# Optimization experiments

Hardware: AMD Instinct MI355X
Metric: run time of the kernel (lower is better)

The kernel has to match this reference:

```python
import jax, jax.numpy as jnp
import numpy as np

N_NODES = 50000
N_EDGES = 800000
IN, HID, OUT = 128, 128, 64


def _mean_agg(h, src, dst, n):
    # gather source-node features along edges, segment-mean into destination nodes
    msgs = h[src]                                          # [E, d]
    summ = jax.ops.segment_sum(msgs, dst, num_segments=n)  # [N, d]
    deg = jax.ops.segment_sum(jnp.ones((src.shape[0],), h.dtype), dst, num_segments=n)
    return summ / jnp.maximum(deg, 1.0)[:, None]           # zero-in-degree -> 0


def _sage_layer(h, src, dst, W_self, W_neigh, b, n):
    # DGL SAGEConv mean: fc_self(h) + fc_neigh(mean_neigh(h)) + bias
    agg = _mean_agg(h, src, dst, n)
    return h @ W_self + agg @ W_neigh + b


def setup_inputs() -> dict:
    key = jax.random.key(0)
    ks = jax.random.split(key, 8)
    s = 1.0 / np.sqrt(IN)
    return {
        "feat": jax.random.normal(ks[0], (N_NODES, IN), jnp.float32),
        "src": jax.random.randint(ks[1], (N_EDGES,), 0, N_NODES, jnp.int64),
        "dst": jax.random.randint(ks[2], (N_EDGES,), 0, N_NODES, jnp.int64),
        "W_self1": jax.random.normal(ks[3], (IN, HID), jnp.float32) * s,
        "W_neigh1": jax.random.normal(ks[4], (IN, HID), jnp.float32) * s,
        "b1": jnp.zeros((HID,), jnp.float32),
        "W_self2": jax.random.normal(ks[5], (HID, OUT), jnp.float32) * (1.0 / np.sqrt(HID)),
        "W_neigh2": jax.random.normal(ks[6], (HID, OUT), jnp.float32) * (1.0 / np.sqrt(HID)),
        "b2": jnp.zeros((OUT,), jnp.float32),
    }


def reference(feat, src, dst, W_self1, W_neigh1, b1, W_self2, W_neigh2, b2):
    n = feat.shape[0]
    h = _sage_layer(feat, src, dst, W_self1, W_neigh1, b1, n)
    h = jax.nn.relu(h)  # dropout is identity in eval mode
    h = _sage_layer(h, src, dst, W_self2, W_neigh2, b2, n)
    return h
```

## Files before the change

### kernel.cpp

```cpp
#include <hip/hip_runtime.h>

#define N_NODES 50000
#define N_EDGES 800000

typedef unsigned short ushort_t;
typedef unsigned int uint_t;
typedef __attribute__((ext_vector_type(8))) short bf16x8;
typedef __attribute__((ext_vector_type(4))) float f32x4;

#define NB 196
#define BCAP 6144
#define SDEPTH 16
#define EPB 1024
#define NBLK_BUCKET ((N_EDGES + EPB - 1) / EPB)

#define IOFF_ROWPTR  100000
#define IOFF_EIDX    150016
#define IOFF_BBASE   950016
#define IOFF_BCNT    950528
#define UOFF_WT      1920000
#define UOFF_FEATB   2000000
#define UOFF_AGG1B   8400000
#define UOFF_H1B     14800000
#define UOFF_P2B     21200000

__device__ __forceinline__ float bf2f(uint_t u) {
    return __uint_as_float(u << 16);
}
__device__ __forceinline__ uint_t f2bf(float f) {
    uint_t x = __float_as_uint(f);
    return (x + 0x7FFFu + ((x >> 16) & 1u)) >> 16;
}

__global__ __launch_bounds__(256) void bucket_kernel(const int* __restrict__ src,
                                                     const int* __restrict__ dst,
                                                     uint_t* __restrict__ bucket,
                                                     int* __restrict__ bcnt) {
    __shared__ uint_t stage[NB][SDEPTH];
    __shared__ int lcnt[NB];
    __shared__ int gbase[NB];
    int tid = threadIdx.x;
    for (int i = tid; i < NB; i += 256) lcnt[i] = 0;
    __syncthreads();
    int e0 = blockIdx.x * EPB;
#pragma unroll
    for (int it = 0; it < EPB / 256; ++it) {
        int e = e0 + it * 256 + tid;
        if (e < N_EDGES) {
            int d = dst[e], s = src[e];
            uint_t v = ((uint_t)d << 16) | (uint_t)s;
            int b = d >> 8;
            int slot = atomicAdd(&lcnt[b], 1);
            if (slot < SDEPTH) {
                stage[b][slot] = v;
            } else {
                int p = atomicAdd(&bcnt[b], 1);
                bucket[(long)b * BCAP + p] = v;
            }
        }
    }
    __syncthreads();
    if (tid < NB) {
        int n = min(lcnt[tid], SDEPTH);
        gbase[tid] = (n > 0) ? atomicAdd(&bcnt[tid], n) : 0;
    }
    __syncthreads();
    for (int s = tid; s < NB * SDEPTH; s += 256) {
        int b = s >> 4, i = s & (SDEPTH - 1);
        if (i < min(lcnt[b], SDEPTH))
            bucket[(long)b * BCAP + gbase[b] + i] = stage[b][i];
    }
}

__global__ __launch_bounds__(256) void scan196(const int* __restrict__ bcnt,
                                               int* __restrict__ bbase,
                                               int* __restrict__ rowptr) {
    __shared__ int sh[256];
    int tid = threadIdx.x;
    int v = (tid < NB) ? bcnt[tid] : 0;
    sh[tid] = v;
    __syncthreads();
    for (int off = 1; off < 256; off <<= 1) {
        int t = (tid >= off) ? sh[tid - off] : 0;
        __syncthreads();
        sh[tid] += t;
        __syncthreads();
    }
    if (tid < NB) bbase[tid] = sh[tid] - v;
    if (tid == NB - 1) rowptr[N_NODES] = sh[tid];
}

__global__ __launch_bounds__(512) void fill_bucket(const uint_t* __restrict__ bucket,
                                                   const int* __restrict__ bcnt,
                                                   const int* __restrict__ bbase,
                                                   int* __restrict__ rowptr,
                                                   int* __restrict__ eidx) {
    __shared__ int hist[256];
    __shared__ int excl[256];
    __shared__ int fp[256];
    int b = blockIdx.x, tid = threadIdx.x;
    if (tid < 256) { hist[tid] = 0; fp[tid] = 0; }
    __syncthreads();
    int n = bcnt[b];
    int base = bbase[b];
    int nodebase = b << 8;
    const uint_t* bk = bucket + (long)b * BCAP;
    for (int i = tid; i < n; i += 512) {
        int d = (int)(bk[i] >> 16) - nodebase;
        atomicAdd(&hist[d], 1);
    }
    __syncthreads();
    int v = 0;
    if (tid < 256) { v = hist[tid]; excl[tid] = v; }
    __syncthreads();
    for (int off = 1; off < 256; off <<= 1) {
        int t = 0;
        if (tid < 256 && tid >= off) t = excl[tid - off];
        __syncthreads();
        if (tid < 256) excl[tid] += t;
        __syncthreads();
    }
    if (tid < 256) {
        excl[tid] -= v;
        int node = nodebase + tid;
        if (node < N_NODES) rowptr[node] = base + excl[tid];
    }
    __syncthreads();
    for (int i = tid; i < n; i += 512) {
        uint_t vv = bk[i];
        int d = (int)(vv >> 16) - nodebase;
        int off = atomicAdd(&fp[d], 1);
        eidx[base + excl[d] + off] = (int)(vv & 0xFFFFu);
    }
}

__global__ __launch_bounds__(256) void cvt_kernel(const float* __restrict__ x,
                                                  ushort_t* __restrict__ y, int n4) {
    int i = blockIdx.x * 256 + threadIdx.x;
    if (i >= n4) return;
    float4 v = ((const float4*)x)[i];
    uint2 o;
    o.x = f2bf(v.x) | (f2bf(v.y) << 16);
    o.y = f2bf(v.z) | (f2bf(v.w) << 16);
    ((uint2*)y)[i] = o;
}

__global__ __launch_bounds__(256) void wprep_kernel(const float* __restrict__ Ws1,
                                                    const float* __restrict__ Wn1,
                                                    const float* __restrict__ Ws2,
                                                    const float* __restrict__ Wn2,
                                                    ushort_t* __restrict__ wT) {
    int i = blockIdx.x * 256 + threadIdx.x;
    if (i >= 49152) return;
    float v;
    if (i < 16384) {
        int n = i >> 7, k = i & 127;
        v = Ws1[k * 128 + n];
    } else if (i < 32768) {
        int j = i - 16384, n = j >> 7, k = j & 127;
        v = Wn1[k * 128 + n];
    } else if (i < 40960) {
        int j = i - 32768, n = j >> 7, k = j & 127;
        v = Wn2[k * 64 + n];
    } else {
        int j = i - 40960, n = j >> 7, k = j & 127;
        v = Ws2[k * 64 + n];
    }
    wT[i] = (ushort_t)f2bf(v);
}

__global__ __launch_bounds__(256) void gather128_kernel(const int* __restrict__ rowptr,
                                                        const int* __restrict__ eidx,
                                                        const ushort_t* __restrict__ xb,
                                                        ushort_t* __restrict__ aggb) {
    int node = blockIdx.x * 4 + (threadIdx.x >> 6);
    int lane = threadIdx.x & 63;
    if (node >= N_NODES) return;
    int q = lane >> 4;
    int sl = lane & 15;
    int beg = rowptr[node], end = rowptr[node + 1];
    float acc[8];
#pragma unroll
    for (int j = 0; j < 8; ++j) acc[j] = 0.f;

    int e = beg;
    for (; e + 7 < end; e += 8) {
        int sA = eidx[e + q];
        int sB = eidx[e + 4 + q];
        uint4 vA = *(const uint4*)(xb + (long)sA * 128 + sl * 8);
        uint4 vB = *(const uint4*)(xb + (long)sB * 128 + sl * 8);
        acc[0] += bf2f(vA.x & 0xffffu); acc[1] += bf2f(vA.x >> 16);
        acc[2] += bf2f(vA.y & 0xffffu); acc[3] += bf2f(vA.y >> 16);
        acc[4] += bf2f(vA.z & 0xffffu); acc[5] += bf2f(vA.z >> 16);
        acc[6] += bf2f(vA.w & 0xffffu); acc[7] += bf2f(vA.w >> 16);
        acc[0] += bf2f(vB.x & 0xffffu); acc[1] += bf2f(vB.x >> 16);
        acc[2] += bf2f(vB.y & 0xffffu); acc[3] += bf2f(vB.y >> 16);
        acc[4] += bf2f(vB.z & 0xffffu); acc[5] += bf2f(vB.z >> 16);
        acc[6] += bf2f(vB.w & 0xffffu); acc[7] += bf2f(vB.w >> 16);
    }
    for (; e + 3 < end; e += 4) {
        int s = eidx[e + q];
        uint4 v = *(const uint4*)(xb + (long)s * 128 + sl * 8);
        acc[0] += bf2f(v.x & 0xffffu); acc[1] += bf2f(v.x >> 16);
        acc[2] += bf2f(v.y & 0xffffu); acc[3] += bf2f(v.y >> 16);
        acc[4] += bf2f(v.z & 0xffffu); acc[5] += bf2f(v.z >> 16);
        acc[6] += bf2f(v.w & 0xffffu); acc[7] += bf2f(v.w >> 16);
    }
    if (e + q < end) {
        int s = eidx[e + q];
        uint4 v = *(const uint4*)(xb + (long)s * 128 + sl * 8);
        acc[0] += bf2f(v.x & 0xffffu); acc[1] += bf2f(v.x >> 16);
        acc[2] += bf2f(v.y & 0xffffu); acc[3] += bf2f(v.y >> 16);
        acc[4] += bf2f(v.z & 0xffffu); acc[5] += bf2f(v.z >> 16);
        acc[6] += bf2f(v.w & 0xffffu); acc[7] += bf2f(v.w >> 16);
    }
#pragma unroll
    for (int j = 0; j < 8; ++j) {
        acc[j] += __shfl_xor(acc[j], 16);
        acc[j] += __shfl_xor(acc[j], 32);
    }
    float inv = (end > beg) ? 1.0f / (float)(end - beg) : 0.f;
    if (lane < 16) {
        uint4 o;
        o.x = f2bf(acc[0] * inv) | (f2bf(acc[1] * inv) << 16);
        o.y = f2bf(acc[2] * inv) | (f2bf(acc[3] * inv) << 16);
        o.z = f2bf(acc[4] * inv) | (f2bf(acc[5] * inv) << 16);
        o.w = f2bf(acc[6] * inv) | (f2bf(acc[7] * inv) << 16);
        *(uint4*)(aggb + (long)node * 128 + sl * 8) = o;
    }
}

__global__ __launch_bounds__(256) void gather64_add_kernel(const int* __restrict__ rowptr,
                                                           const int* __restrict__ eidx,
                                                           const ushort_t* __restrict__ p2b,
                                                           float* __restrict__ out) {
    int node = blockIdx.x * 4 + (threadIdx.x >> 6);
    int lane = threadIdx.x & 63;
    if (node >= N_NODES) return;
    int q = lane >> 4;
    int sl = lane & 15;
    int beg = rowptr[node], end = rowptr[node + 1];
    float acc[4];
#pragma unroll
    for (int j = 0; j < 4; ++j) acc[j] = 0.f;

    int e = beg;
    for (; e + 7 < end; e += 8) {
        int sA = eidx[e + q];
        int sB = eidx[e + 4 + q];
        uint2 vA = *(const uint2*)(p2b + (long)sA * 64 + sl * 4);
        uint2 vB = *(const uint2*)(p2b + (long)sB * 64 + sl * 4);
        acc[0] += bf2f(vA.x & 0xffffu); acc[1] += bf2f(vA.x >> 16);
        acc[2] += bf2f(vA.y & 0xffffu); acc[3] += bf2f(vA.y >> 16);
        acc[0] += bf2f(vB.x & 0xffffu); acc[1] += bf2f(vB.x >> 16);
        acc[2] += bf2f(vB.y & 0xffffu); acc[3] += bf2f(vB.y >> 16);
    }
    for (; e + 3 < end; e += 4) {
        int s = eidx[e + q];
        uint2 v = *(const uint2*)(p2b + (long)s * 64 + sl * 4);
        acc[0] += bf2f(v.x & 0xffffu); acc[1] += bf2f(v.x >> 16);
        acc[2] += bf2f(v.y & 0xffffu); acc[3] += bf2f(v.y >> 16);
    }
    if (e + q < end) {
        int s = eidx[e + q];
        uint2 v = *(const uint2*)(p2b + (long)s * 64 + sl * 4);
        acc[0] += bf2f(v.x & 0xffffu); acc[1] += bf2f(v.x >> 16);
        acc[2] += bf2f(v.y & 0xffffu); acc[3] += bf2f(v.y >> 16);
    }
#pragma unroll
    for (int j = 0; j < 4; ++j) {
        acc[j] += __shfl_xor(acc[j], 16);
        acc[j] += __shfl_xor(acc[j], 32);
    }
    float inv = (end > beg) ? 1.0f / (float)(end - beg) : 0.f;
    if (lane < 16) {
        float4* po = (float4*)(out + (long)node * 64 + sl * 4);
        float4 o = *po;
        o.x += acc[0] * inv;
        o.y += acc[1] * inv;
        o.z += acc[2] * inv;
        o.w += acc[3] * inv;
        *po = o;
    }
}


__global__ __launch_bounds__(256) void gemm1_mfma(const ushort_t* __restrict__ featb,
                                                  const ushort_t* __restrict__ agg1b,
                                                  const ushort_t* __restrict__ wT,
                                                  const float* __restrict__ b,
                                                  ushort_t* __restrict__ h1b) {
    int lane = threadIdx.x & 63;
    int w = threadIdx.x >> 6;
    int mbase = blockIdx.x * 128 + w * 32;
    int lr = lane & 15;
    int kg = (lane >> 4) * 8;

    long r0 = mbase + lr;
    long r1 = mbase + 16 + lr;
    if (r0 > N_NODES - 1) r0 = N_NODES - 1;
    if (r1 > N_NODES - 1) r1 = N_NODES - 1;

    f32x4 acc[2][8];
#pragma unroll
    for (int mt = 0; mt < 2; ++mt)
#pragma unroll
        for (int nt = 0; nt < 8; ++nt) acc[mt][nt] = (f32x4){0.f, 0.f, 0.f, 0.f};

#pragma unroll
    for (int pass = 0; pass < 2; ++pass) {
        const ushort_t* a = pass ? agg1b : featb;
        const ushort_t* wt = wT + pass * (128 * 128);
#pragma unroll
        for (int ks = 0; ks < 4; ++ks) {
            int k = ks * 32 + kg;
            bf16x8 a0 = *(const bf16x8*)(a + r0 * 128 + k);
            bf16x8 a1 = *(const bf16x8*)(a + r1 * 128 + k);
#pragma unroll
            for (int nt = 0; nt < 8; ++nt) {
                bf16x8 bb = *(const bf16x8*)(wt + (nt * 16 + lr) * 128 + k);
                acc[0][nt] = __builtin_amdgcn_mfma_f32_16x16x32_bf16(a0, bb, acc[0][nt], 0, 0, 0);
                acc[1][nt] = __builtin_amdgcn_mfma_f32_16x16x32_bf16(a1, bb, acc[1][nt], 0, 0, 0);
            }
        }
    }

    int drow = (lane >> 4) * 4;
#pragma unroll
    for (int nt = 0; nt < 8; ++nt) {
        int n = nt * 16 + lr;
        float bias = b[n];
#pragma unroll
        for (int mt = 0; mt < 2; ++mt) {
#pragma unroll
            for (int r = 0; r < 4; ++r) {
                int row = mbase + mt * 16 + drow + r;
                if (row < N_NODES) {
                    float v = fmaxf(acc[mt][nt][r] + bias, 0.f);
                    h1b[(long)row * 128 + n] = (ushort_t)f2bf(v);
                }
            }
        }
    }
}

__global__ __launch_bounds__(256) void gemm2_mfma(const ushort_t* __restrict__ h1b,
                                                  const ushort_t* __restrict__ wT2,
                                                  const float* __restrict__ b2,
                                                  ushort_t* __restrict__ p2b,
                                                  float* __restrict__ out) {
    int lane = threadIdx.x & 63;
    int w = threadIdx.x >> 6;
    int mbase = blockIdx.x * 128 + w * 32;
    int lr = lane & 15;
    int kg = (lane >> 4) * 8;

    long r0 = mbase + lr;
    long r1 = mbase + 16 + lr;
    if (r0 > N_NODES - 1) r0 = N_NODES - 1;
    if (r1 > N_NODES - 1) r1 = N_NODES - 1;

    f32x4 accP[2][4], accO[2][4];
#pragma unroll
    for (int mt = 0; mt < 2; ++mt)
#pragma unroll
        for (int nt = 0; nt < 4; ++nt) {
            accP[mt][nt] = (f32x4){0.f, 0.f, 0.f, 0.f};
            accO[mt][nt] = (f32x4){0.f, 0.f, 0.f, 0.f};
        }

#pragma unroll
    for (int ks = 0; ks < 4; ++ks) {
        int k = ks * 32 + kg;
        bf16x8 a0 = *(const bf16x8*)(h1b + r0 * 128 + k);
        bf16x8 a1 = *(const bf16x8*)(h1b + r1 * 128 + k);
#pragma unroll
        for (int nt = 0; nt < 4; ++nt) {
            bf16x8 bn = *(const bf16x8*)(wT2 + (nt * 16 + lr) * 128 + k);
            bf16x8 bs = *(const bf16x8*)(wT2 + 8192 + (nt * 16 + lr) * 128 + k);
            accP[0][nt] = __builtin_amdgcn_mfma_f32_16x16x32_bf16(a0, bn, accP[0][nt], 0, 0, 0);
            accP[1][nt] = __builtin_amdgcn_mfma_f32_16x16x32_bf16(a1, bn, accP[1][nt], 0, 0, 0);
            accO[0][nt] = __builtin_amdgcn_mfma_f32_16x16x32_bf16(a0, bs, accO[0][nt], 0, 0, 0);
            accO[1][nt] = __builtin_amdgcn_mfma_f32_16x16x32_bf16(a1, bs, accO[1][nt], 0, 0, 0);
        }
    }

    int drow = (lane >> 4) * 4;
#pragma unroll
    for (int nt = 0; nt < 4; ++nt) {
        int n = nt * 16 + lr;
        float bias = b2[n];
#pragma unroll
        for (int mt = 0; mt < 2; ++mt) {
#pragma unroll
            for (int r = 0; r < 4; ++r) {
                int row = mbase + mt * 16 + drow + r;
                if (row < N_NODES) {
                    p2b[(long)row * 64 + n] = (ushort_t)f2bf(accP[mt][nt][r]);
                    out[(long)row * 64 + n] = accO[mt][nt][r] + bias;
                }
            }
        }
    }
}

extern "C" void kernel_launch(void* const* d_in, const int* in_sizes, int n_in,
                              void* d_out, int out_size, void* d_ws, size_t ws_size,
                              hipStream_t stream) {
    const float* feat = (const float*)d_in[0];
    const int* src    = (const int*)d_in[1];
    const int* dst    = (const int*)d_in[2];
    const float* Ws1  = (const float*)d_in[3];
    const float* Wn1  = (const float*)d_in[4];
    const float* b1   = (const float*)d_in[5];
    const float* Ws2  = (const float*)d_in[6];
    const float* Wn2  = (const float*)d_in[7];
    const float* b2   = (const float*)d_in[8];
    float* out = (float*)d_out;

    int* wsi      = (int*)d_ws;
    ushort_t* wsu = (ushort_t*)d_ws;
    int* rowptr   = wsi + IOFF_ROWPTR;
    int* eidx     = wsi + IOFF_EIDX;
    int* bbase    = wsi + IOFF_BBASE;
    int* bcnt     = wsi + IOFF_BCNT;
    ushort_t* wT    = wsu + UOFF_WT;
    ushort_t* featb = wsu + UOFF_FEATB;
    ushort_t* agg1b = wsu + UOFF_AGG1B;
    ushort_t* h1b   = wsu + UOFF_H1B;
    ushort_t* p2b   = wsu + UOFF_P2B;
    uint_t* bucket  = (uint_t*)(wsu + UOFF_H1B);

    hipMemsetAsync(bcnt, 0, NB * sizeof(int), stream);

    wprep_kernel<<<(49152 + 255) / 256, 256, 0, stream>>>(Ws1, Wn1, Ws2, Wn2, wT);
    cvt_kernel<<<(N_NODES * 128 / 4 + 255) / 256, 256, 0, stream>>>(feat, featb, N_NODES * 128 / 4);

    bucket_kernel<<<NBLK_BUCKET, 256, 0, stream>>>(src, dst, bucket, bcnt);
    scan196<<<1, 256, 0, stream>>>(bcnt, bbase, rowptr);
    fill_bucket<<<NB, 512, 0, stream>>>(bucket, bcnt, bbase, rowptr, eidx);

    gather128_kernel<<<(N_NODES + 3) / 4, 256, 0, stream>>>(rowptr, eidx, featb, agg1b);
    gemm1_mfma<<<(N_NODES + 127) / 128, 256, 0, stream>>>(featb, agg1b, wT, b1, h1b);

    gemm2_mfma<<<(N_NODES + 127) / 128, 256, 0, stream>>>(h1b, wT + 32768, b2, p2b, out);
    gather64_add_kernel<<<(N_NODES + 3) / 4, 256, 0, stream>>>(rowptr, eidx, p2b, out);
}
```

Baseline: 224.7 us.

## Merge prep kernels, fold bucket scan into fill, use 16-bit edge indices

```diff
diff --git a/kernel.cpp b/kernel.cpp
--- a/kernel.cpp
+++ b/kernel.cpp
@@ -10,13 +10,13 @@
 
 #define NB 196
 #define BCAP 6144
-#define SDEPTH 16
-#define EPB 1024
+#define SDEPTH 32
+#define EPB 2048
 #define NBLK_BUCKET ((N_EDGES + EPB - 1) / EPB)
+#define NCVT4 (N_NODES * 128 / 4)
 
 #define IOFF_ROWPTR  100000
 #define IOFF_EIDX    150016
-#define IOFF_BBASE   950016
 #define IOFF_BCNT    950528
 #define UOFF_WT      1920000
 #define UOFF_FEATB   2000000
@@ -30,6 +30,46 @@
 __device__ __forceinline__ uint_t f2bf(float f) {
     uint_t x = __float_as_uint(f);
     return (x + 0x7FFFu + ((x >> 16) & 1u)) >> 16;
+}
+
+__global__ __launch_bounds__(256) void prep_kernel(const float* __restrict__ feat,
+                                                   const float* __restrict__ Ws1,
+                                                   const float* __restrict__ Wn1,
+                                                   const float* __restrict__ Ws2,
+                                                   const float* __restrict__ Wn2,
+                                                   ushort_t* __restrict__ featb,
+                                                   ushort_t* __restrict__ wT,
+                                                   int* __restrict__ bcnt) {
+    int i = blockIdx.x * 256 + threadIdx.x;
+    if (i < NCVT4) {
+        float4 v = ((const float4*)feat)[i];
+        uint2 o;
+        o.x = f2bf(v.x) | (f2bf(v.y) << 16);
+        o.y = f2bf(v.z) | (f2bf(v.w) << 16);
+        ((uint2*)featb)[i] = o;
+        return;
+    }
+    int j = i - NCVT4;
+    if (j < 49152) {
+        float v;
+        if (j < 16384) {
+            int n = j >> 7, k = j & 127;
+            v = Ws1[k * 128 + n];
+        } else if (j < 32768) {
+            int jj = j - 16384, n = jj >> 7, k = jj & 127;
+            v = Wn1[k * 128 + n];
+        } else if (j < 40960) {
+            int jj = j - 32768, n = jj >> 7, k = jj & 127;
+            v = Wn2[k * 64 + n];
+        } else {
+            int jj = j - 40960, n = jj >> 7, k = jj & 127;
+            v = Ws2[k * 64 + n];
+        }
+        wT[j] = (ushort_t)f2bf(v);
+        return;
+    }
+    int z = j - 49152;
+    if (z < NB) bcnt[z] = 0;
 }
 
 __global__ __launch_bounds__(256) void bucket_kernel(const int* __restrict__ src,
@@ -66,46 +106,40 @@
     }
     __syncthreads();
     for (int s = tid; s < NB * SDEPTH; s += 256) {
-        int b = s >> 4, i = s & (SDEPTH - 1);
+        int b = s >> 5, i = s & (SDEPTH - 1);
         if (i < min(lcnt[b], SDEPTH))
             bucket[(long)b * BCAP + gbase[b] + i] = stage[b][i];
     }
 }
 
-__global__ __launch_bounds__(256) void scan196(const int* __restrict__ bcnt,
-                                               int* __restrict__ bbase,
-                                               int* __restrict__ rowptr) {
-    __shared__ int sh[256];
-    int tid = threadIdx.x;
-    int v = (tid < NB) ? bcnt[tid] : 0;
-    sh[tid] = v;
-    __syncthreads();
-    for (int off = 1; off < 256; off <<= 1) {
-        int t = (tid >= off) ? sh[tid - off] : 0;
-        __syncthreads();
-        sh[tid] += t;
-        __syncthreads();
-    }
-    if (tid < NB) bbase[tid] = sh[tid] - v;
-    if (tid == NB - 1) rowptr[N_NODES] = sh[tid];
-}
-
-__global__ __launch_bounds__(512) void fill_bucket(const uint_t* __restrict__ bucket,
-                                                   const int* __restrict__ bcnt,
-                                                   const int* __restrict__ bbase,
-                                                   int* __restrict__ rowptr,
-                                                   int* __restrict__ eidx) {
+__global__ __launch_bounds__(1024) void fill_bucket(const uint_t* __restrict__ bucket,
+                                                    const int* __restrict__ bcnt,
+                                                    int* __restrict__ rowptr,
+                                                    ushort_t* __restrict__ eidx) {
+    __shared__ int pref[256];
     __shared__ int hist[256];
     __shared__ int excl[256];
     __shared__ int fp[256];
     int b = blockIdx.x, tid = threadIdx.x;
-    if (tid < 256) { hist[tid] = 0; fp[tid] = 0; }
-    __syncthreads();
+    if (tid < 256) {
+        pref[tid] = (tid < NB) ? bcnt[tid] : 0;
+        hist[tid] = 0;
+        fp[tid] = 0;
+    }
+    __syncthreads();
+    for (int off = 1; off < 256; off <<= 1) {
+        int t = 0;
+        if (tid < 256 && tid >= off) t = pref[tid - off];
+        __syncthreads();
+        if (tid < 256) pref[tid] += t;
+        __syncthreads();
+    }
     int n = bcnt[b];
-    int base = bbase[b];
+    int base = pref[b] - n;
+    if (b == NB - 1 && tid == 0) rowptr[N_NODES] = pref[NB - 1];
     int nodebase = b << 8;
     const uint_t* bk = bucket + (long)b * BCAP;
-    for (int i = tid; i < n; i += 512) {
+    for (int i = tid; i < n; i += 1024) {
         int d = (int)(bk[i] >> 16) - nodebase;
         atomicAdd(&hist[d], 1);
     }
@@ -126,51 +160,16 @@
         if (node < N_NODES) rowptr[node] = base + excl[tid];
     }
     __syncthreads();
-    for (int i = tid; i < n; i += 512) {
+    for (int i = tid; i < n; i += 1024) {
         uint_t vv = bk[i];
         int d = (int)(vv >> 16) - nodebase;
         int off = atomicAdd(&fp[d], 1);
-        eidx[base + excl[d] + off] = (int)(vv & 0xFFFFu);
-    }
-}
-
-__global__ __launch_bounds__(256) void cvt_kernel(const float* __restrict__ x,
-                                                  ushort_t* __restrict__ y, int n4) {
-    int i = blockIdx.x * 256 + threadIdx.x;
-    if (i >= n4) return;
-    float4 v = ((const float4*)x)[i];
-    uint2 o;
-    o.x = f2bf(v.x) | (f2bf(v.y) << 16);
-    o.y = f2bf(v.z) | (f2bf(v.w) << 16);
-    ((uint2*)y)[i] = o;
-}
-
-__global__ __launch_bounds__(256) void wprep_kernel(const float* __restrict__ Ws1,
-                                                    const float* __restrict__ Wn1,
-                                                    const float* __restrict__ Ws2,
-                                                    const float* __restrict__ Wn2,
-                                                    ushort_t* __restrict__ wT) {
-    int i = blockIdx.x * 256 + threadIdx.x;
-    if (i >= 49152) return;
-    float v;
-    if (i < 16384) {
-        int n = i >> 7, k = i & 127;
-        v = Ws1[k * 128 + n];
-    } else if (i < 32768) {
-        int j = i - 16384, n = j >> 7, k = j & 127;
-        v = Wn1[k * 128 + n];
-    } else if (i < 40960) {
-        int j = i - 32768, n = j >> 7, k = j & 127;
-        v = Wn2[k * 64 + n];
-    } else {
-        int j = i - 40960, n = j >> 7, k = j & 127;
-        v = Ws2[k * 64 + n];
-    }
-    wT[i] = (ushort_t)f2bf(v);
+        eidx[base + excl[d] + off] = (ushort_t)(vv & 0xFFFFu);
+    }
 }
 
 __global__ __launch_bounds__(256) void gather128_kernel(const int* __restrict__ rowptr,
-                                                        const int* __restrict__ eidx,
+                                                        const ushort_t* __restrict__ eidx,
                                                         const ushort_t* __restrict__ xb,
                                                         ushort_t* __restrict__ aggb) {
     int node = blockIdx.x * 4 + (threadIdx.x >> 6);
@@ -231,7 +230,7 @@
 }
 
 __global__ __launch_bounds__(256) void gather64_add_kernel(const int* __restrict__ rowptr,
-                                                           const int* __restrict__ eidx,
+                                                           const ushort_t* __restrict__ eidx,
                                                            const ushort_t* __restrict__ p2b,
                                                            float* __restrict__ out) {
     int node = blockIdx.x * 4 + (threadIdx.x >> 6);
@@ -420,10 +419,9 @@
 
     int* wsi      = (int*)d_ws;
     ushort_t* wsu = (ushort_t*)d_ws;
-    int* rowptr   = wsi + IOFF_ROWPTR;
-    int* eidx     = wsi + IOFF_EIDX;
-    int* bbase    = wsi + IOFF_BBASE;
-    int* bcnt     = wsi + IOFF_BCNT;
+    int* rowptr       = wsi + IOFF_ROWPTR;
+    ushort_t* eidx    = (ushort_t*)(wsi + IOFF_EIDX);
+    int* bcnt         = wsi + IOFF_BCNT;
     ushort_t* wT    = wsu + UOFF_WT;
     ushort_t* featb = wsu + UOFF_FEATB;
     ushort_t* agg1b = wsu + UOFF_AGG1B;
@@ -431,14 +429,11 @@
     ushort_t* p2b   = wsu + UOFF_P2B;
     uint_t* bucket  = (uint_t*)(wsu + UOFF_H1B);
 
-    hipMemsetAsync(bcnt, 0, NB * sizeof(int), stream);
-
-    wprep_kernel<<<(49152 + 255) / 256, 256, 0, stream>>>(Ws1, Wn1, Ws2, Wn2, wT);
-    cvt_kernel<<<(N_NODES * 128 / 4 + 255) / 256, 256, 0, stream>>>(feat, featb, N_NODES * 128 / 4);
+    prep_kernel<<<(NCVT4 + 49152 + NB + 255) / 256, 256, 0, stream>>>(
+        feat, Ws1, Wn1, Ws2, Wn2, featb, wT, bcnt);
 
     bucket_kernel<<<NBLK_BUCKET, 256, 0, stream>>>(src, dst, bucket, bcnt);
-    scan196<<<1, 256, 0, stream>>>(bcnt, bbase, rowptr);
-    fill_bucket<<<NB, 512, 0, stream>>>(bucket, bcnt, bbase, rowptr, eidx);
+    fill_bucket<<<NB, 1024, 0, stream>>>(bucket, bcnt, rowptr, eidx);
 
     gather128_kernel<<<(N_NODES + 3) / 4, 256, 0, stream>>>(rowptr, eidx, featb, agg1b);
     gemm1_mfma<<<(N_NODES + 127) / 128, 256, 0, stream>>>(featb, agg1b, wT, b1, h1b);
```

After: 213.5 us. 1.05x faster.
